# Performance work log

Measured on AMD Instinct MI355X. Metric: run time of the kernel, lower is better.

The kernel has to match this reference:

```python
import jax, jax.numpy as jnp
import numpy as np

D_MODEL = 1024
N_HEADS = 16
HEAD_DIM = D_MODEL // N_HEADS


def setup_inputs() -> dict:
    key = jax.random.key(0)
    k0, k1, k2, k3, k4, k5 = jax.random.split(key, 6)
    s = 1.0 / np.sqrt(D_MODEL)
    return {
        "q": jax.random.normal(k0, (2, 2048, D_MODEL), dtype=jnp.float32),
        "Wq": jax.random.normal(k1, (D_MODEL, D_MODEL), dtype=jnp.float32) * s,
        "Wk": jax.random.normal(k2, (D_MODEL, D_MODEL), dtype=jnp.float32) * s,
        "Wv": jax.random.normal(k3, (D_MODEL, D_MODEL), dtype=jnp.float32) * s,
        "Wo": jax.random.normal(k4, (D_MODEL, D_MODEL), dtype=jnp.float32) * s,
        "bo": jax.random.normal(k5, (D_MODEL,), dtype=jnp.float32) * 0.01,
    }


def _split_heads(x):
    b, s, _ = x.shape
    return x.reshape(b, s, N_HEADS, HEAD_DIM).transpose(0, 2, 1, 3)  # [b,h,s,d]


def reference(q, Wq, Wk, Wv, Wo, bo):
    # self-attention: k = v = q
    qh = _split_heads(q @ Wq)  # [b,h,s,d]
    kh = _split_heads(q @ Wk)
    vh = _split_heads(q @ Wv)
    scale = 1.0 / np.sqrt(HEAD_DIM).astype(np.float32)
    scores = jnp.einsum("bhqd,bhkd->bhqk", qh, kh) * scale
    attn = jax.nn.softmax(scores, axis=-1)
    ctx = jnp.einsum("bhqk,bhkd->bhqd", attn, vh)
    b, h, s, d = ctx.shape
    ctx = ctx.transpose(0, 2, 1, 3).reshape(b, s, h * d)
    return ctx @ Wo + bo
```

## Files before the change

### kernel.cpp

```cpp
#include <hip/hip_runtime.h>
#include <cstdint>

typedef unsigned short u16;
typedef __bf16 bf16x8 __attribute__((ext_vector_type(8)));
typedef __bf16 bf16x2 __attribute__((ext_vector_type(2)));
typedef float floatx4 __attribute__((ext_vector_type(4)));
typedef unsigned short u16x4 __attribute__((ext_vector_type(4)));
typedef unsigned short u16x8 __attribute__((ext_vector_type(8)));

#define MFMA16(a, b, c) __builtin_amdgcn_mfma_f32_16x16x32_bf16((a), (b), (c), 0, 0, 0)
#define QSCALE_LOG2E 0.18033688011112042f


typedef __attribute__((address_space(3))) void as3_void;
typedef __attribute__((address_space(1))) void as1_void;

static __device__ __forceinline__ void async_load16(const void* g, void* l) {
  __builtin_amdgcn_global_load_lds((as1_void*)(uintptr_t)g, (as3_void*)(uintptr_t)l,
                                   16, 0, 0);
}

static __device__ __forceinline__ u16 f2bf(float f) {
  union { float f; unsigned int u; } v; v.f = f;
  unsigned int u = v.u;
  u += 0x7fffu + ((u >> 16) & 1u);
  return (u16)(u >> 16);
}

static __device__ __forceinline__ u16x4 pack_bf4(float a, float b, float c, float d) {
#if __has_builtin(__builtin_amdgcn_cvt_pk_bf16_f32)
  union { u16x4 v4; bf16x2 v2[2]; } u;
  u.v2[0] = __builtin_amdgcn_cvt_pk_bf16_f32(a, b);
  u.v2[1] = __builtin_amdgcn_cvt_pk_bf16_f32(c, d);
  return u.v4;
#else
  u16x4 r; r[0] = f2bf(a); r[1] = f2bf(b); r[2] = f2bf(c); r[3] = f2bf(d);
  return r;
#endif
}

static __device__ __forceinline__ unsigned pack_bf2(float a, float b) {
#if __has_builtin(__builtin_amdgcn_cvt_pk_bf16_f32)
  union { bf16x2 v; unsigned u; } x;
  x.v = __builtin_amdgcn_cvt_pk_bf16_f32(a, b);
  return x.u;
#else
  return (unsigned)f2bf(a) | ((unsigned)f2bf(b) << 16);
#endif
}

static __device__ __forceinline__ float fast_exp2(float x) {
#if __has_builtin(__builtin_amdgcn_exp2f)
  return __builtin_amdgcn_exp2f(x);
#else
  return exp2f(x);
#endif
}


__global__ __launch_bounds__(256) void prep_kernel(
    const float* __restrict__ w0, const float* __restrict__ w1,
    const float* __restrict__ w2, const float* __restrict__ w3,
    u16* __restrict__ wout,
    const float* __restrict__ xin, u16* __restrict__ xout) {
  if (blockIdx.z == 4) {
    int blk = blockIdx.y * 16 + blockIdx.x;
    size_t base = (size_t)blk * 16384 + (size_t)threadIdx.x * 8;
#pragma unroll
    for (int r = 0; r < 8; r++) {
      size_t i = base + (size_t)r * 2048;
      float4 a = *(const float4*)(xin + i);
      float4 b = *(const float4*)(xin + i + 4);
      u16x8 o;
      o[0] = f2bf(a.x); o[1] = f2bf(a.y); o[2] = f2bf(a.z); o[3] = f2bf(a.w);
      o[4] = f2bf(b.x); o[5] = f2bf(b.y); o[6] = f2bf(b.z); o[7] = f2bf(b.w);
      *(u16x8*)(xout + i) = o;
    }
    return;
  }
  __shared__ u16 t[64][65];
  const float* in = (blockIdx.z == 0) ? w0 : (blockIdx.z == 1) ? w1
                    : (blockIdx.z == 2) ? w2 : w3;
  u16* oz = wout + (size_t)blockIdx.z * (1024 * 1024);
  const int tid = threadIdx.x;
  const int x = tid & 63, y0 = tid >> 6;
  const int bx = blockIdx.x * 64, by = blockIdx.y * 64;
#pragma unroll
  for (int p = 0; p < 16; p++) {
    int y = y0 + p * 4;
    t[y][x] = f2bf(in[(size_t)(by + y) * 1024 + bx + x]);
  }
  __syncthreads();
#pragma unroll
  for (int p = 0; p < 16; p++) {
    int r = y0 + p * 4;
    oz[(size_t)(bx + r) * 1024 + by + x] = t[x][r];
  }
}


__global__ __launch_bounds__(256, 3) void gemm_qkv_kernel(
    const u16* __restrict__ A, const u16* __restrict__ BT,
    u16* __restrict__ out, u16* __restrict__ outVT) {
  __shared__ u16 As[2 * 4096];
  __shared__ u16 Bs[2 * 4096];
  __shared__ u16 tb[64 * 136];
  const int tid = threadIdx.x;
  const int w = tid >> 6, lane = tid & 63;
  const int bm = blockIdx.y * 128, bn = blockIdx.x * 128;
  const int z = blockIdx.z;
  const int K = 1024, N = 1024;
  const u16* Bz = BT + (size_t)z * N * K;

  const int c0 = w * 2, c1 = c0 + 1;
  const int mA0 = c0 * 16 + (lane >> 2), mA1 = c1 * 16 + (lane >> 2);
  const int kg0 = (lane & 3) ^ ((mA0 >> 1) & 3);
  const int kg1 = (lane & 3) ^ ((mA1 >> 1) & 3);
  const u16* agp0 = A + (size_t)(bm + mA0) * K + kg0 * 8;
  const u16* agp1 = A + (size_t)(bm + mA1) * K + kg1 * 8;
  const u16* bgp0 = Bz + (size_t)(bn + mA0) * K + kg0 * 8;
  const u16* bgp1 = Bz + (size_t)(bn + mA1) * K + kg1 * 8;

  const int wm = (w >> 1) * 64, wn = (w & 1) * 64;
  floatx4 acc[4][4] = {};

  int a_off[4], b_off[4];
#pragma unroll
  for (int i = 0; i < 4; i++) {
    int m = wm + i * 16 + (lane & 15);
    a_off[i] = m * 32 + (((lane >> 4) ^ ((m >> 1) & 3)) * 8);
    int n = wn + i * 16 + (lane & 15);
    b_off[i] = n * 32 + (((lane >> 4) ^ ((n >> 1) & 3)) * 8);
  }

  auto issueQ = [&](int buf, int k0) {
    u16* ab = As + buf * 4096;
    u16* bb = Bs + buf * 4096;
    async_load16(agp0 + k0, ab + c0 * 512);
    async_load16(agp1 + k0, ab + c1 * 512);
    async_load16(bgp0 + k0, bb + c0 * 512);
    async_load16(bgp1 + k0, bb + c1 * 512);
  };

  issueQ(0, 0);
  asm volatile("s_waitcnt vmcnt(0)" ::: "memory");
  __builtin_amdgcn_s_barrier();

#pragma unroll 2
  for (int kk = 0; kk < 32; ++kk) {
    if (kk < 31) issueQ((kk + 1) & 1, (kk + 1) * 32);
    const u16* Ab = As + (kk & 1) * 4096;
    const u16* Bb = Bs + (kk & 1) * 4096;
    bf16x8 af[4], bf[4];
#pragma unroll
    for (int i = 0; i < 4; i++) af[i] = *(const bf16x8*)(Ab + a_off[i]);
#pragma unroll
    for (int j = 0; j < 4; j++) bf[j] = *(const bf16x8*)(Bb + b_off[j]);
#pragma unroll
    for (int i = 0; i < 4; i++)
#pragma unroll
      for (int j = 0; j < 4; j++)
        acc[i][j] = MFMA16(af[i], bf[j], acc[i][j]);
    asm volatile("s_waitcnt vmcnt(0) lgkmcnt(0)" ::: "memory");
    __builtin_amdgcn_s_barrier();
  }

  const int roff = (lane >> 4) * 4;
  const int coff = lane & 15;
  if (z == 2) {
    const int b = bm >> 11, s0 = bm & 2047;
#pragma unroll
    for (int half = 0; half < 2; half++) {
      __syncthreads();
      if ((w & 1) == half) {
#pragma unroll
        for (int i = 0; i < 4; i++) {
          int s_local = wm + i * 16 + roff;
#pragma unroll
          for (int j = 0; j < 4; j++) {
            int c_local = j * 16 + coff;
            u16x4 pk = pack_bf4(acc[i][j][0], acc[i][j][1],
                                acc[i][j][2], acc[i][j][3]);
            *(u16x4*)(tb + c_local * 136 + s_local) = pk;
          }
        }
      }
      __syncthreads();
#pragma unroll
      for (int p = 0; p < 4; p++) {
        int c_local = (tid >> 4) & 15;
        int row = p * 16 + c_local;
        int so = tid & 15;
        int cg = bn + half * 64 + row;
        int h = cg >> 6, d = cg & 63;
        u16x8 vv = *(const u16x8*)(tb + row * 136 + so * 8);
        *(u16x8*)(outVT + ((size_t)(b * 16 + h) * 64 + d) * 2048 + s0 + so * 8) = vv;
      }
    }
  } else {
    const float sc = (z == 0) ? QSCALE_LOG2E : 1.0f;
    u16* outz = out + (size_t)z * 4096 * 1024;
#pragma unroll
    for (int i = 0; i < 4; i++) {
      int r0 = bm + wm + i * 16 + roff;
#pragma unroll
      for (int j = 0; j < 4; j++) {
        int c = bn + wn + j * 16 + coff;
#pragma unroll
        for (int r = 0; r < 4; r++)
          outz[(size_t)(r0 + r) * N + c] = f2bf(acc[i][j][r] * sc);
      }
    }
  }
}


__global__ __launch_bounds__(256, 2) void gemm_o_kernel(
    const u16* __restrict__ A, const u16* __restrict__ BT,
    const float* __restrict__ bias, float* __restrict__ out) {
  __shared__ u16 As[2 * 4096];
  __shared__ u16 Bs[2 * 2048];
  const int tid = threadIdx.x;
  const int w = tid >> 6, lane = tid & 63;
  const int bm = blockIdx.y * 128, bn = blockIdx.x * 64;
  const int K = 1024, N = 1024;

  const u16* gp[3];
  u16* ldp[2][3];
#pragma unroll
  for (int i = 0; i < 3; i++) {
    int c = w * 3 + i;
    if (c < 8) {
      int m = c * 16 + (lane >> 2);
      int kg = (lane & 3) ^ ((m >> 1) & 3);
      gp[i] = A + (size_t)(bm + m) * K + kg * 8;
      ldp[0][i] = As + c * 512;
      ldp[1][i] = As + 4096 + c * 512;
    } else {
      int cb = c - 8;
      int n = cb * 16 + (lane >> 2);
      int kg = (lane & 3) ^ ((n >> 1) & 3);
      gp[i] = BT + (size_t)(bn + n) * K + kg * 8;
      ldp[0][i] = Bs + cb * 512;
      ldp[1][i] = Bs + 2048 + cb * 512;
    }
  }

  const int wm = (w >> 1) * 64, wn = (w & 1) * 32;
  floatx4 acc[4][2] = {};

  int a_off[4], b_off[2];
#pragma unroll
  for (int i = 0; i < 4; i++) {
    int m = wm + i * 16 + (lane & 15);
    a_off[i] = m * 32 + (((lane >> 4) ^ ((m >> 1) & 3)) * 8);
  }
#pragma unroll
  for (int j = 0; j < 2; j++) {
    int n = wn + j * 16 + (lane & 15);
    b_off[j] = n * 32 + (((lane >> 4) ^ ((n >> 1) & 3)) * 8);
  }

  auto issueO = [&](int buf, int k0) {
#pragma unroll
    for (int i = 0; i < 3; i++)
      async_load16(gp[i] + k0, buf ? ldp[1][i] : ldp[0][i]);
  };

  issueO(0, 0);
  asm volatile("s_waitcnt vmcnt(0)" ::: "memory");
  __builtin_amdgcn_s_barrier();

#pragma unroll 2
  for (int kk = 0; kk < 32; ++kk) {
    if (kk < 31) issueO((kk + 1) & 1, (kk + 1) * 32);
    const u16* Ab = As + (kk & 1) * 4096;
    const u16* Bb = Bs + (kk & 1) * 2048;
    bf16x8 af[4], bf[2];
#pragma unroll
    for (int i = 0; i < 4; i++) af[i] = *(const bf16x8*)(Ab + a_off[i]);
#pragma unroll
    for (int j = 0; j < 2; j++) bf[j] = *(const bf16x8*)(Bb + b_off[j]);
#pragma unroll
    for (int i = 0; i < 4; i++)
#pragma unroll
      for (int j = 0; j < 2; j++)
        acc[i][j] = MFMA16(af[i], bf[j], acc[i][j]);
    asm volatile("s_waitcnt vmcnt(0) lgkmcnt(0)" ::: "memory");
    __builtin_amdgcn_s_barrier();
  }

  const int roff = (lane >> 4) * 4;
  const int coff = lane & 15;
#pragma unroll
  for (int i = 0; i < 4; i++) {
    int r0 = bm + wm + i * 16 + roff;
#pragma unroll
    for (int j = 0; j < 2; j++) {
      int c = bn + wn + j * 16 + coff;
      float bv = bias[c];
#pragma unroll
      for (int r = 0; r < 4; r++)
        out[(size_t)(r0 + r) * N + c] = acc[i][j][r] + bv;
    }
  }
}


__global__ __launch_bounds__(512, 4) void attn_kernel(
    const u16* __restrict__ Q, const u16* __restrict__ Kx,
    const u16* __restrict__ VT, u16* __restrict__ ctx) {
  __shared__ __align__(16) u16 lds[32768];
  const int tid = threadIdx.x;
  const int w = tid >> 6, lane = tid & 63;
  const int qq = w >> 1, sh = w & 1;
  const int quad = lane >> 4;
  const int bid = blockIdx.x;
  const int bh = (bid >> 7) * 8 + (bid & 7);
  const int q0 = ((bid >> 3) & 15) * 128;
  const int b = bh >> 4, h = bh & 15;
  const u16* Qh = Q + (size_t)b * 2048 * 1024 + h * 64;
  const u16* Kh = Kx + (size_t)b * 2048 * 1024 + h * 64;
  const u16* Vh = VT + (size_t)bh * 64 * 2048;

  {
    u16x8 z8 = {};
    *(u16x8*)(lds + 24576 + tid * 8) = z8;
    *(u16x8*)(lds + 24576 + 4096 + tid * 8) = z8;
  }

  const u16* kgp[2]; const u16* vgp[2];
  int kc[2], vc[2];
#pragma unroll
  for (int i = 0; i < 2; i++) {
    int c = w * 2 + i;
    int sl = c * 8 + (lane >> 3);
    int dg = (lane & 7) ^ (lane >> 3);
    kgp[i] = Kh + (size_t)sl * 1024 + dg * 8;
    kc[i] = c * 512;
    int dl = c * 4 + quad;
    int sg = (lane & 15) ^ (dl & 15);
    vgp[i] = Vh + (size_t)dl * 2048 + sg * 8;
    vc[i] = 8192 + c * 512;
  }

  auto issue_tile = [&](int buf, int t) {
    u16* dst = lds + buf * 16384;
    const size_t k0 = (size_t)t * 128;
#pragma unroll
    for (int i = 0; i < 2; i++) {
      async_load16(kgp[i] + k0 * 1024, dst + kc[i]);
      async_load16(vgp[i] + k0, dst + vc[i]);
    }
  };

  issue_tile(0, 0);

  const int qbase = q0 + qq * 32;
  bf16x8 qf[2][2];
#pragma unroll
  for (int qt = 0; qt < 2; qt++)
#pragma unroll
    for (int ks = 0; ks < 2; ks++)
      qf[qt][ks] = *(const bf16x8*)(Qh + (size_t)(qbase + qt * 16 + (lane & 15)) * 1024 +
                                    ks * 32 + quad * 8);

  bf16x8 onesf;
#pragma unroll
  for (int i = 0; i < 8; i++) onesf[i] = (__bf16)1.0f;
  const floatx4 zero4 = {};

  const int slot_k0 = quad ^ (lane & 7);
  const int slot_k1 = (4 + quad) ^ (lane & 7);
  const int koff0 = sh * 4096 + (lane & 15) * 64 + slot_k0 * 8;
  const int koff1 = sh * 4096 + (lane & 15) * 64 + slot_k1 * 8;
  const int sq = ((quad & 1) << 1) | (quad >> 1);
  int vf_off[2][4];
#pragma unroll
  for (int ksl = 0; ksl < 2; ksl++)
#pragma unroll
    for (int jt = 0; jt < 4; jt++) {
      int d = jt * 16 + (lane & 15);
      int kb = sh * 2 + ksl;
      int slot = (kb * 4 + sq) ^ (d & 15);
      vf_off[ksl][jt] = d * 128 + slot * 8;
    }

  floatx4 o[2][4] = {};
  floatx4 lacc[2] = {};
  bf16x8 pf_prev[2][2];
#pragma unroll
  for (int a = 0; a < 2; a++)
#pragma unroll
    for (int c = 0; c < 2; c++) pf_prev[a][c] = bf16x8{};

  asm volatile("s_waitcnt vmcnt(0)" ::: "memory");
  __builtin_amdgcn_s_barrier();

#pragma unroll 2
  for (int t = 0; t < 16; ++t) {
    const u16* Ksb = lds + (t & 1) * 16384;
    const u16* Vsb_prev = lds + ((t + 1) & 1) * 16384 + 8192;

    bf16x8 vf[2][4];
#pragma unroll
    for (int ksl = 0; ksl < 2; ksl++)
#pragma unroll
      for (int jt = 0; jt < 4; jt++)
        vf[ksl][jt] = *(const bf16x8*)(Vsb_prev + vf_off[ksl][jt]);
    asm volatile("s_waitcnt lgkmcnt(0)" ::: "memory");
    __builtin_amdgcn_sched_barrier(0);
    __builtin_amdgcn_s_barrier();
    if (t < 15) issue_tile((t + 1) & 1, t + 1);

#pragma unroll
    for (int ksl = 0; ksl < 2; ksl++)
#pragma unroll
      for (int qt = 0; qt < 2; qt++) {
#pragma unroll
        for (int jt = 0; jt < 4; jt++)
          o[qt][jt] = MFMA16(pf_prev[qt][ksl], vf[ksl][jt], o[qt][jt]);
        lacc[qt] = MFMA16(pf_prev[qt][ksl], onesf, lacc[qt]);
      }

    floatx4 st[4][2];
#pragma unroll
    for (int si = 0; si < 4; si++) {
      bf16x8 kf0 = *(const bf16x8*)(Ksb + koff0 + si * 1024);
      bf16x8 kf1 = *(const bf16x8*)(Ksb + koff1 + si * 1024);
#pragma unroll
      for (int qt = 0; qt < 2; qt++)
        st[si][qt] = MFMA16(kf1, qf[qt][1], MFMA16(kf0, qf[qt][0], zero4));
    }

    unsigned pa[2][4], pb[2][4];
#pragma unroll
    for (int si = 0; si < 4; si++)
#pragma unroll
      for (int qt = 0; qt < 2; qt++) {
        pa[qt][si] = pack_bf2(fast_exp2(st[si][qt][0]), fast_exp2(st[si][qt][1]));
        pb[qt][si] = pack_bf2(fast_exp2(st[si][qt][2]), fast_exp2(st[si][qt][3]));
      }

#pragma unroll
    for (int qt = 0; qt < 2; qt++)
#pragma unroll
      for (int ksl = 0; ksl < 2; ksl++) {
        unsigned x0 = pa[qt][2 * ksl], x1 = pa[qt][2 * ksl + 1];
        unsigned y0 = pb[qt][2 * ksl], y1 = pb[qt][2 * ksl + 1];
        asm("v_permlane16_swap_b32 %0, %1" : "+v"(x0), "+v"(x1));
        asm("v_permlane16_swap_b32 %0, %1" : "+v"(y0), "+v"(y1));
        union { unsigned u[4]; bf16x8 v; } uu;
        uu.u[0] = x0; uu.u[1] = y0; uu.u[2] = x1; uu.u[3] = y1;
        pf_prev[qt][ksl] = uu.v;
      }

    asm volatile("s_waitcnt vmcnt(0)" ::: "memory");
  }

  {
    const u16* Vsb = lds + 16384 + 8192;
    bf16x8 vf[2][4];
#pragma unroll
    for (int ksl = 0; ksl < 2; ksl++)
#pragma unroll
      for (int jt = 0; jt < 4; jt++)
        vf[ksl][jt] = *(const bf16x8*)(Vsb + vf_off[ksl][jt]);
#pragma unroll
    for (int ksl = 0; ksl < 2; ksl++)
#pragma unroll
      for (int qt = 0; qt < 2; qt++) {
#pragma unroll
        for (int jt = 0; jt < 4; jt++)
          o[qt][jt] = MFMA16(pf_prev[qt][ksl], vf[ksl][jt], o[qt][jt]);
        lacc[qt] = MFMA16(pf_prev[qt][ksl], onesf, lacc[qt]);
      }
  }

  __syncthreads();
  floatx4* dump  = (floatx4*)lds;
  floatx4* ldump = (floatx4*)(lds + 16384);
  if (sh == 1) {
    int base = qq * 512;
#pragma unroll
    for (int qt = 0; qt < 2; qt++)
#pragma unroll
      for (int jt = 0; jt < 4; jt++)
        dump[base + (qt * 4 + jt) * 64 + lane] = o[qt][jt];
#pragma unroll
    for (int qt = 0; qt < 2; qt++)
      ldump[qq * 128 + qt * 64 + lane] = lacc[qt];
  }
  __syncthreads();
  if (sh == 0) {
    int base = qq * 512;
#pragma unroll
    for (int qt = 0; qt < 2; qt++)
#pragma unroll
      for (int jt = 0; jt < 4; jt++)
        o[qt][jt] += dump[base + (qt * 4 + jt) * 64 + lane];
#pragma unroll
    for (int qt = 0; qt < 2; qt++)
      lacc[qt] += ldump[qq * 128 + qt * 64 + lane];
#pragma unroll
    for (int qt = 0; qt < 2; qt++)
#pragma unroll
      for (int r = 0; r < 4; r++) {
        float inv = 1.0f / lacc[qt][r];
        int s = qbase + qt * 16 + quad * 4 + r;
#pragma unroll
        for (int j = 0; j < 4; j++) {
          int c = h * 64 + j * 16 + (lane & 15);
          ctx[(size_t)(b * 2048 + s) * 1024 + c] = f2bf(o[qt][j][r] * inv);
        }
      }
  }
}


extern "C" void kernel_launch(void* const* d_in, const int* in_sizes, int n_in,
                              void* d_out, int out_size, void* d_ws, size_t ws_size,
                              hipStream_t stream) {
  (void)in_sizes; (void)n_in; (void)out_size; (void)ws_size;
  const float* x  = (const float*)d_in[0];
  const float* Wq = (const float*)d_in[1];
  const float* Wk = (const float*)d_in[2];
  const float* Wv = (const float*)d_in[3];
  const float* Wo = (const float*)d_in[4];
  const float* bo = (const float*)d_in[5];
  u16* ws = (u16*)d_ws;
  const size_t MM = 1024 * 1024;
  u16* WT  = ws;
  u16* WoT = ws + 3 * MM;
  u16* Xb  = ws + 4 * MM;
  u16* QKV = ws + 8 * MM;
  u16* VTp = ws + 20 * MM;
  u16* CTX = ws + 24 * MM;

  dim3 blk(256);
  prep_kernel<<<dim3(16, 16, 5), blk, 0, stream>>>(Wq, Wk, Wv, Wo, WT, x, Xb);
  gemm_qkv_kernel<<<dim3(8, 32, 3), blk, 0, stream>>>(Xb, WT, QKV, VTp);
  attn_kernel<<<dim3(512, 1, 1), dim3(512), 0, stream>>>(QKV, QKV + 4 * MM, VTp, CTX);
  gemm_o_kernel<<<dim3(16, 32, 1), blk, 0, stream>>>(CTX, WoT, bo, (float*)d_out);
}
```

Baseline: 205.4 us.

## Split attention key tiles across four waves per query group with 1024-thread blocks

Doubles the attention block to 16 waves, so each query group's 128-key tile is split four ways instead of two, with one async load per thread per tile. The software pipeline that overlapped the previous tile's PV matmul with the next tile's QK is removed, and PV now runs in the same iteration. The cross-wave reduction becomes three sequential LDS rounds with extra barriers. This trades more parallelism and shorter per-wave work for lost intra-wave overlap, more barriers, and 1024-thread launch bounds that may limit registers per thread.

```diff
diff --git a/kernel.cpp b/kernel.cpp
--- a/kernel.cpp
+++ b/kernel.cpp
@@ -307,13 +307,13 @@
 }
 
 
-__global__ __launch_bounds__(512, 4) void attn_kernel(
+__global__ __launch_bounds__(1024, 8) void attn_kernel(
     const u16* __restrict__ Q, const u16* __restrict__ Kx,
     const u16* __restrict__ VT, u16* __restrict__ ctx) {
   __shared__ __align__(16) u16 lds[32768];
   const int tid = threadIdx.x;
   const int w = tid >> 6, lane = tid & 63;
-  const int qq = w >> 1, sh = w & 1;
+  const int qq = w >> 2, sh = w & 3;
   const int quad = lane >> 4;
   const int bid = blockIdx.x;
   const int bh = (bid >> 7) * 8 + (bid & 7);
@@ -323,35 +323,20 @@
   const u16* Kh = Kx + (size_t)b * 2048 * 1024 + h * 64;
   const u16* Vh = VT + (size_t)bh * 64 * 2048;
 
-  {
-    u16x8 z8 = {};
-    *(u16x8*)(lds + 24576 + tid * 8) = z8;
-    *(u16x8*)(lds + 24576 + 4096 + tid * 8) = z8;
-  }
-
-  const u16* kgp[2]; const u16* vgp[2];
-  int kc[2], vc[2];
-#pragma unroll
-  for (int i = 0; i < 2; i++) {
-    int c = w * 2 + i;
-    int sl = c * 8 + (lane >> 3);
-    int dg = (lane & 7) ^ (lane >> 3);
-    kgp[i] = Kh + (size_t)sl * 1024 + dg * 8;
-    kc[i] = c * 512;
-    int dl = c * 4 + quad;
-    int sg = (lane & 15) ^ (dl & 15);
-    vgp[i] = Vh + (size_t)dl * 2048 + sg * 8;
-    vc[i] = 8192 + c * 512;
-  }
+  const int sl = w * 8 + (lane >> 3);
+  const int dg = (lane & 7) ^ (lane >> 3);
+  const u16* kgp = Kh + (size_t)sl * 1024 + dg * 8;
+  const int kc = w * 512;
+  const int dl = w * 4 + quad;
+  const int sg = (lane & 15) ^ (dl & 15);
+  const u16* vgp = Vh + (size_t)dl * 2048 + sg * 8;
+  const int vc = 8192 + w * 512;
 
   auto issue_tile = [&](int buf, int t) {
     u16* dst = lds + buf * 16384;
     const size_t k0 = (size_t)t * 128;
-#pragma unroll
-    for (int i = 0; i < 2; i++) {
-      async_load16(kgp[i] + k0 * 1024, dst + kc[i]);
-      async_load16(vgp[i] + k0, dst + vc[i]);
-    }
+    async_load16(kgp + k0 * 1024, dst + kc);
+    async_load16(vgp + k0, dst + vc);
   };
 
   issue_tile(0, 0);
@@ -370,62 +355,33 @@
   for (int i = 0; i < 8; i++) onesf[i] = (__bf16)1.0f;
   const floatx4 zero4 = {};
 
-  const int slot_k0 = quad ^ (lane & 7);
-  const int slot_k1 = (4 + quad) ^ (lane & 7);
-  const int koff0 = sh * 4096 + (lane & 15) * 64 + slot_k0 * 8;
-  const int koff1 = sh * 4096 + (lane & 15) * 64 + slot_k1 * 8;
+  const int koff0 = (sh * 32 + (lane & 15)) * 64 + ((quad ^ (lane & 7)) * 8);
+  const int koff1 = (sh * 32 + (lane & 15)) * 64 + (((4 + quad) ^ (lane & 7)) * 8);
   const int sq = ((quad & 1) << 1) | (quad >> 1);
-  int vf_off[2][4];
-#pragma unroll
-  for (int ksl = 0; ksl < 2; ksl++)
-#pragma unroll
-    for (int jt = 0; jt < 4; jt++) {
-      int d = jt * 16 + (lane & 15);
-      int kb = sh * 2 + ksl;
-      int slot = (kb * 4 + sq) ^ (d & 15);
-      vf_off[ksl][jt] = d * 128 + slot * 8;
-    }
+  int vf_off[4];
+#pragma unroll
+  for (int jt = 0; jt < 4; jt++) {
+    int d = jt * 16 + (lane & 15);
+    int slot = (sh * 4 + sq) ^ (d & 15);
+    vf_off[jt] = d * 128 + slot * 8;
+  }
 
   floatx4 o[2][4] = {};
   floatx4 lacc[2] = {};
-  bf16x8 pf_prev[2][2];
-#pragma unroll
-  for (int a = 0; a < 2; a++)
-#pragma unroll
-    for (int c = 0; c < 2; c++) pf_prev[a][c] = bf16x8{};
 
   asm volatile("s_waitcnt vmcnt(0)" ::: "memory");
-  __builtin_amdgcn_s_barrier();
 
 #pragma unroll 2
   for (int t = 0; t < 16; ++t) {
+    __builtin_amdgcn_s_barrier();
+    __builtin_amdgcn_sched_barrier(0);
+    if (t < 15) issue_tile((t + 1) & 1, t + 1);
     const u16* Ksb = lds + (t & 1) * 16384;
-    const u16* Vsb_prev = lds + ((t + 1) & 1) * 16384 + 8192;
-
-    bf16x8 vf[2][4];
-#pragma unroll
-    for (int ksl = 0; ksl < 2; ksl++)
-#pragma unroll
-      for (int jt = 0; jt < 4; jt++)
-        vf[ksl][jt] = *(const bf16x8*)(Vsb_prev + vf_off[ksl][jt]);
-    asm volatile("s_waitcnt lgkmcnt(0)" ::: "memory");
-    __builtin_amdgcn_sched_barrier(0);
-    __builtin_amdgcn_s_barrier();
-    if (t < 15) issue_tile((t + 1) & 1, t + 1);
-
-#pragma unroll
-    for (int ksl = 0; ksl < 2; ksl++)
-#pragma unroll
-      for (int qt = 0; qt < 2; qt++) {
-#pragma unroll
-        for (int jt = 0; jt < 4; jt++)
-          o[qt][jt] = MFMA16(pf_prev[qt][ksl], vf[ksl][jt], o[qt][jt]);
-        lacc[qt] = MFMA16(pf_prev[qt][ksl], onesf, lacc[qt]);
-      }
-
-    floatx4 st[4][2];
-#pragma unroll
-    for (int si = 0; si < 4; si++) {
+    const u16* Vsb = Ksb + 8192;
+
+    floatx4 st[2][2];
+#pragma unroll
+    for (int si = 0; si < 2; si++) {
       bf16x8 kf0 = *(const bf16x8*)(Ksb + koff0 + si * 1024);
       bf16x8 kf1 = *(const bf16x8*)(Ksb + koff1 + si * 1024);
 #pragma unroll
@@ -433,75 +389,71 @@
         st[si][qt] = MFMA16(kf1, qf[qt][1], MFMA16(kf0, qf[qt][0], zero4));
     }
 
-    unsigned pa[2][4], pb[2][4];
-#pragma unroll
-    for (int si = 0; si < 4; si++)
+    unsigned pa[2][2], pb[2][2];
+#pragma unroll
+    for (int si = 0; si < 2; si++)
 #pragma unroll
       for (int qt = 0; qt < 2; qt++) {
         pa[qt][si] = pack_bf2(fast_exp2(st[si][qt][0]), fast_exp2(st[si][qt][1]));
         pb[qt][si] = pack_bf2(fast_exp2(st[si][qt][2]), fast_exp2(st[si][qt][3]));
       }
 
-#pragma unroll
-    for (int qt = 0; qt < 2; qt++)
-#pragma unroll
-      for (int ksl = 0; ksl < 2; ksl++) {
-        unsigned x0 = pa[qt][2 * ksl], x1 = pa[qt][2 * ksl + 1];
-        unsigned y0 = pb[qt][2 * ksl], y1 = pb[qt][2 * ksl + 1];
-        asm("v_permlane16_swap_b32 %0, %1" : "+v"(x0), "+v"(x1));
-        asm("v_permlane16_swap_b32 %0, %1" : "+v"(y0), "+v"(y1));
-        union { unsigned u[4]; bf16x8 v; } uu;
-        uu.u[0] = x0; uu.u[1] = y0; uu.u[2] = x1; uu.u[3] = y1;
-        pf_prev[qt][ksl] = uu.v;
-      }
-
+    bf16x8 pf[2];
+#pragma unroll
+    for (int qt = 0; qt < 2; qt++) {
+      unsigned x0 = pa[qt][0], x1 = pa[qt][1];
+      unsigned y0 = pb[qt][0], y1 = pb[qt][1];
+      asm("v_permlane16_swap_b32 %0, %1" : "+v"(x0), "+v"(x1));
+      asm("v_permlane16_swap_b32 %0, %1" : "+v"(y0), "+v"(y1));
+      union { unsigned u[4]; bf16x8 v; } uu;
+      uu.u[0] = x0; uu.u[1] = y0; uu.u[2] = x1; uu.u[3] = y1;
+      pf[qt] = uu.v;
+    }
+
+    bf16x8 vf[4];
+#pragma unroll
+    for (int jt = 0; jt < 4; jt++)
+      vf[jt] = *(const bf16x8*)(Vsb + vf_off[jt]);
+#pragma unroll
+    for (int qt = 0; qt < 2; qt++) {
+#pragma unroll
+      for (int jt = 0; jt < 4; jt++)
+        o[qt][jt] = MFMA16(pf[qt], vf[jt], o[qt][jt]);
+      lacc[qt] = MFMA16(pf[qt], onesf, lacc[qt]);
+    }
     asm volatile("s_waitcnt vmcnt(0)" ::: "memory");
   }
 
-  {
-    const u16* Vsb = lds + 16384 + 8192;
-    bf16x8 vf[2][4];
-#pragma unroll
-    for (int ksl = 0; ksl < 2; ksl++)
-#pragma unroll
-      for (int jt = 0; jt < 4; jt++)
-        vf[ksl][jt] = *(const bf16x8*)(Vsb + vf_off[ksl][jt]);
-#pragma unroll
-    for (int ksl = 0; ksl < 2; ksl++)
-#pragma unroll
-      for (int qt = 0; qt < 2; qt++) {
-#pragma unroll
-        for (int jt = 0; jt < 4; jt++)
-          o[qt][jt] = MFMA16(pf_prev[qt][ksl], vf[ksl][jt], o[qt][jt]);
-        lacc[qt] = MFMA16(pf_prev[qt][ksl], onesf, lacc[qt]);
-      }
-  }
-
-  __syncthreads();
   floatx4* dump  = (floatx4*)lds;
   floatx4* ldump = (floatx4*)(lds + 16384);
-  if (sh == 1) {
-    int base = qq * 512;
-#pragma unroll
-    for (int qt = 0; qt < 2; qt++)
-#pragma unroll
-      for (int jt = 0; jt < 4; jt++)
-        dump[base + (qt * 4 + jt) * 64 + lane] = o[qt][jt];
-#pragma unroll
-    for (int qt = 0; qt < 2; qt++)
-      ldump[qq * 128 + qt * 64 + lane] = lacc[qt];
-  }
-  __syncthreads();
+#pragma unroll
+  for (int p = 1; p < 4; p++) {
+    __syncthreads();
+    if (sh == p) {
+      int base = qq * 512;
+#pragma unroll
+      for (int qt = 0; qt < 2; qt++)
+#pragma unroll
+        for (int jt = 0; jt < 4; jt++)
+          dump[base + (qt * 4 + jt) * 64 + lane] = o[qt][jt];
+#pragma unroll
+      for (int qt = 0; qt < 2; qt++)
+        ldump[qq * 128 + qt * 64 + lane] = lacc[qt];
+    }
+    __syncthreads();
+    if (sh == 0) {
+      int base = qq * 512;
+#pragma unroll
+      for (int qt = 0; qt < 2; qt++)
+#pragma unroll
+        for (int jt = 0; jt < 4; jt++)
+          o[qt][jt] += dump[base + (qt * 4 + jt) * 64 + lane];
+#pragma unroll
+      for (int qt = 0; qt < 2; qt++)
+        lacc[qt] += ldump[qq * 128 + qt * 64 + lane];
+    }
+  }
   if (sh == 0) {
-    int base = qq * 512;
-#pragma unroll
-    for (int qt = 0; qt < 2; qt++)
-#pragma unroll
-      for (int jt = 0; jt < 4; jt++)
-        o[qt][jt] += dump[base + (qt * 4 + jt) * 64 + lane];
-#pragma unroll
-    for (int qt = 0; qt < 2; qt++)
-      lacc[qt] += ldump[qq * 128 + qt * 64 + lane];
 #pragma unroll
     for (int qt = 0; qt < 2; qt++)
 #pragma unroll
@@ -540,6 +492,6 @@
   dim3 blk(256);
   prep_kernel<<<dim3(16, 16, 5), blk, 0, stream>>>(Wq, Wk, Wv, Wo, WT, x, Xb);
   gemm_qkv_kernel<<<dim3(8, 32, 3), blk, 0, stream>>>(Xb, WT, QKV, VTp);
-  attn_kernel<<<dim3(512, 1, 1), dim3(512), 0, stream>>>(QKV, QKV + 4 * MM, VTp, CTX);
+  attn_kernel<<<dim3(512, 1, 1), dim3(1024), 0, stream>>>(QKV, QKV + 4 * MM, VTp, CTX);
   gemm_o_kernel<<<dim3(16, 32, 1), blk, 0, stream>>>(CTX, WoT, bo, (float*)d_out);
 }
```

After: 423.5 us. +106.2%, slower.

## Un-skew attention PV pipeline, add MFMA priority hints, alias GEMM LDS buffers

Applied to the files above, without the earlier changes.

The attention loop no longer defers the P·V MFMAs to the next iteration. Each tile now computes QK^T, exp and P·V in sequence from the same buffer, which removes the pf_prev carry, the tail epilogue and the LDS zero-init. s_setprio(1) is raised around the MFMA blocks in the QKV GEMM, the output GEMM and the attention loop, so waves in the matrix phase get issue priority. The QKV GEMM also aliases its transpose scratch buffer onto the A/B staging buffers to cut LDS use per block, which may allow more resident blocks. The trade-off is less overlap between V-fragment LDS reads and QK MFMAs inside a wave, which now relies on cross-wave interleaving instead.

```diff
diff --git a/kernel.cpp b/kernel.cpp
--- a/kernel.cpp
+++ b/kernel.cpp
@@ -102,9 +102,10 @@
 __global__ __launch_bounds__(256, 3) void gemm_qkv_kernel(
     const u16* __restrict__ A, const u16* __restrict__ BT,
     u16* __restrict__ out, u16* __restrict__ outVT) {
-  __shared__ u16 As[2 * 4096];
-  __shared__ u16 Bs[2 * 4096];
-  __shared__ u16 tb[64 * 136];
+  __shared__ __align__(16) u16 sm[2 * 4096 + 2 * 4096];
+  u16* As = sm;
+  u16* Bs = sm + 2 * 4096;
+  u16* tb = sm;
   const int tid = threadIdx.x;
   const int w = tid >> 6, lane = tid & 63;
   const int bm = blockIdx.y * 128, bn = blockIdx.x * 128;
@@ -156,11 +157,13 @@
     for (int i = 0; i < 4; i++) af[i] = *(const bf16x8*)(Ab + a_off[i]);
 #pragma unroll
     for (int j = 0; j < 4; j++) bf[j] = *(const bf16x8*)(Bb + b_off[j]);
+    __builtin_amdgcn_s_setprio(1);
 #pragma unroll
     for (int i = 0; i < 4; i++)
 #pragma unroll
       for (int j = 0; j < 4; j++)
         acc[i][j] = MFMA16(af[i], bf[j], acc[i][j]);
+    __builtin_amdgcn_s_setprio(0);
     asm volatile("s_waitcnt vmcnt(0) lgkmcnt(0)" ::: "memory");
     __builtin_amdgcn_s_barrier();
   }
@@ -281,11 +284,13 @@
     for (int i = 0; i < 4; i++) af[i] = *(const bf16x8*)(Ab + a_off[i]);
 #pragma unroll
     for (int j = 0; j < 2; j++) bf[j] = *(const bf16x8*)(Bb + b_off[j]);
+    __builtin_amdgcn_s_setprio(1);
 #pragma unroll
     for (int i = 0; i < 4; i++)
 #pragma unroll
       for (int j = 0; j < 2; j++)
         acc[i][j] = MFMA16(af[i], bf[j], acc[i][j]);
+    __builtin_amdgcn_s_setprio(0);
     asm volatile("s_waitcnt vmcnt(0) lgkmcnt(0)" ::: "memory");
     __builtin_amdgcn_s_barrier();
   }
@@ -323,12 +328,6 @@
   const u16* Kh = Kx + (size_t)b * 2048 * 1024 + h * 64;
   const u16* Vh = VT + (size_t)bh * 64 * 2048;
 
-  {
-    u16x8 z8 = {};
-    *(u16x8*)(lds + 24576 + tid * 8) = z8;
-    *(u16x8*)(lds + 24576 + 4096 + tid * 8) = z8;
-  }
-
   const u16* kgp[2]; const u16* vgp[2];
   int kc[2], vc[2];
 #pragma unroll
@@ -375,55 +374,22 @@
   const int koff0 = sh * 4096 + (lane & 15) * 64 + slot_k0 * 8;
   const int koff1 = sh * 4096 + (lane & 15) * 64 + slot_k1 * 8;
   const int sq = ((quad & 1) << 1) | (quad >> 1);
-  int vf_off[2][4];
-#pragma unroll
-  for (int ksl = 0; ksl < 2; ksl++)
-#pragma unroll
-    for (int jt = 0; jt < 4; jt++) {
-      int d = jt * 16 + (lane & 15);
-      int kb = sh * 2 + ksl;
-      int slot = (kb * 4 + sq) ^ (d & 15);
-      vf_off[ksl][jt] = d * 128 + slot * 8;
-    }
 
   floatx4 o[2][4] = {};
   floatx4 lacc[2] = {};
-  bf16x8 pf_prev[2][2];
-#pragma unroll
-  for (int a = 0; a < 2; a++)
-#pragma unroll
-    for (int c = 0; c < 2; c++) pf_prev[a][c] = bf16x8{};
 
   asm volatile("s_waitcnt vmcnt(0)" ::: "memory");
-  __builtin_amdgcn_s_barrier();
 
 #pragma unroll 2
   for (int t = 0; t < 16; ++t) {
+    __builtin_amdgcn_s_barrier();
+    __builtin_amdgcn_sched_barrier(0);
+    if (t < 15) issue_tile((t + 1) & 1, t + 1);
     const u16* Ksb = lds + (t & 1) * 16384;
-    const u16* Vsb_prev = lds + ((t + 1) & 1) * 16384 + 8192;
-
-    bf16x8 vf[2][4];
-#pragma unroll
-    for (int ksl = 0; ksl < 2; ksl++)
-#pragma unroll
-      for (int jt = 0; jt < 4; jt++)
-        vf[ksl][jt] = *(const bf16x8*)(Vsb_prev + vf_off[ksl][jt]);
-    asm volatile("s_waitcnt lgkmcnt(0)" ::: "memory");
-    __builtin_amdgcn_sched_barrier(0);
-    __builtin_amdgcn_s_barrier();
-    if (t < 15) issue_tile((t + 1) & 1, t + 1);
-
-#pragma unroll
-    for (int ksl = 0; ksl < 2; ksl++)
-#pragma unroll
-      for (int qt = 0; qt < 2; qt++) {
-#pragma unroll
-        for (int jt = 0; jt < 4; jt++)
-          o[qt][jt] = MFMA16(pf_prev[qt][ksl], vf[ksl][jt], o[qt][jt]);
-        lacc[qt] = MFMA16(pf_prev[qt][ksl], onesf, lacc[qt]);
-      }
+    const u16* Vsb = Ksb + 8192;
 
     floatx4 st[4][2];
+    __builtin_amdgcn_s_setprio(1);
 #pragma unroll
     for (int si = 0; si < 4; si++) {
       bf16x8 kf0 = *(const bf16x8*)(Ksb + koff0 + si * 1024);
@@ -432,6 +398,7 @@
       for (int qt = 0; qt < 2; qt++)
         st[si][qt] = MFMA16(kf1, qf[qt][1], MFMA16(kf0, qf[qt][0], zero4));
     }
+    __builtin_amdgcn_s_setprio(0);
 
     unsigned pa[2][4], pb[2][4];
 #pragma unroll
@@ -442,6 +409,7 @@
         pb[qt][si] = pack_bf2(fast_exp2(st[si][qt][2]), fast_exp2(st[si][qt][3]));
       }
 
+    bf16x8 pf[2][2];
 #pragma unroll
     for (int qt = 0; qt < 2; qt++)
 #pragma unroll
@@ -452,29 +420,30 @@
         asm("v_permlane16_swap_b32 %0, %1" : "+v"(y0), "+v"(y1));
         union { unsigned u[4]; bf16x8 v; } uu;
         uu.u[0] = x0; uu.u[1] = y0; uu.u[2] = x1; uu.u[3] = y1;
-        pf_prev[qt][ksl] = uu.v;
-      }
-
+        pf[qt][ksl] = uu.v;
+      }
+
+    __builtin_amdgcn_s_setprio(1);
+#pragma unroll
+    for (int ksl = 0; ksl < 2; ksl++) {
+      int kb = sh * 2 + ksl;
+      bf16x8 vf[4];
+#pragma unroll
+      for (int jt = 0; jt < 4; jt++) {
+        int d = jt * 16 + (lane & 15);
+        int slot = (kb * 4 + sq) ^ (d & 15);
+        vf[jt] = *(const bf16x8*)(Vsb + d * 128 + slot * 8);
+      }
+#pragma unroll
+      for (int qt = 0; qt < 2; qt++) {
+#pragma unroll
+        for (int jt = 0; jt < 4; jt++)
+          o[qt][jt] = MFMA16(pf[qt][ksl], vf[jt], o[qt][jt]);
+        lacc[qt] = MFMA16(pf[qt][ksl], onesf, lacc[qt]);
+      }
+    }
+    __builtin_amdgcn_s_setprio(0);
     asm volatile("s_waitcnt vmcnt(0)" ::: "memory");
-  }
-
-  {
-    const u16* Vsb = lds + 16384 + 8192;
-    bf16x8 vf[2][4];
-#pragma unroll
-    for (int ksl = 0; ksl < 2; ksl++)
-#pragma unroll
-      for (int jt = 0; jt < 4; jt++)
-        vf[ksl][jt] = *(const bf16x8*)(Vsb + vf_off[ksl][jt]);
-#pragma unroll
-    for (int ksl = 0; ksl < 2; ksl++)
-#pragma unroll
-      for (int qt = 0; qt < 2; qt++) {
-#pragma unroll
-        for (int jt = 0; jt < 4; jt++)
-          o[qt][jt] = MFMA16(pf_prev[qt][ksl], vf[ksl][jt], o[qt][jt]);
-        lacc[qt] = MFMA16(pf_prev[qt][ksl], onesf, lacc[qt]);
-      }
   }
 
   __syncthreads();
```

After: 178.3 us, median of 2. 1.15x faster.
